# Kernel tuning notes

Measured on AMD Instinct MI355X. Metric: run time of the kernel, lower is better.

The kernel has to match this reference:

```python
import jax, jax.numpy as jnp
import numpy as np

NORM = 1.0  # normalization_factor


def _glorot(key, shape):
    fan_in, fan_out = shape
    lim = float(np.sqrt(6.0 / (fan_in + fan_out)))
    return jax.random.uniform(key, shape, jnp.float32, -lim, lim)


def setup_inputs() -> dict:
    key = jax.random.key(0)
    ks = jax.random.split(key, 12)
    B, N = 8, 2048
    latent, hidden, out_dim = 64, 128, 64
    inp = {
        "latent_features": jax.random.normal(ks[0], (B, N, latent), jnp.float32),
        "adjacency_matrix": jax.random.uniform(ks[1], (B, N, N), jnp.float32),
        "node_mask": jnp.ones((B, N, 1), jnp.float32),
        # 3 GCN layers: latent->hidden, hidden->hidden, hidden->hidden
        "W0": _glorot(ks[2], (latent, hidden)), "b0": jnp.zeros((hidden,), jnp.float32),
        "W1": _glorot(ks[3], (hidden, hidden)), "b1": jnp.zeros((hidden,), jnp.float32),
        "W2": _glorot(ks[4], (hidden, hidden)), "b2": jnp.zeros((hidden,), jnp.float32),
        # output projection hidden->out_dim
        "Wout": _glorot(ks[5], (hidden, out_dim)), "bout": jnp.zeros((out_dim,), jnp.float32),
    }
    return inp


def _gcn_layer(h, adj, W, b):
    # message transform (linear), gather+sum aggregate via dense adjacency, ReLU act
    msg = h @ W + b                      # [B,N,dout]
    agg = jnp.einsum('bij,bjd->bid', adj, msg) / NORM  # sum aggregation over neighbors
    return jax.nn.relu(agg)


def reference(latent_features, adjacency_matrix, node_mask,
              W0, b0, W1, b1, W2, b2, Wout, bout):
    h = _gcn_layer(latent_features, adjacency_matrix, W0, b0)
    h = _gcn_layer(h, adjacency_matrix, W1, b1)
    h = _gcn_layer(h, adjacency_matrix, W2, b2)
    # output projection + node mask
    return (h @ Wout + bout) * node_mask
```

## Files before the change

kernel.cpp:

```cpp
#include <hip/hip_runtime.h>
#include <hip/hip_bf16.h>


typedef __bf16 bf16;
typedef __bf16 bf16x4 __attribute__((ext_vector_type(4)));
typedef __bf16 bf16x8 __attribute__((ext_vector_type(8)));
typedef float  f32x16 __attribute__((ext_vector_type(16)));
typedef float  f32x4  __attribute__((ext_vector_type(4)));

static __device__ inline f32x16 mfma32(bf16x8 a, bf16x8 b, f32x16 c) {
    return __builtin_amdgcn_mfma_f32_32x32x16_bf16(a, b, c, 0, 0, 0);
}

#define NB   8
#define NN   2048
#define LAT  64
#define HID  128
#define ODIM 64

__global__ __launch_bounds__(256) void prep_t0_k(
    const float* __restrict__ lat, const float* __restrict__ W0,
    const float* __restrict__ b0,
    const float* __restrict__ W1, const float* __restrict__ W2,
    const float* __restrict__ Wout,
    bf16* __restrict__ msgT, bf16* __restrict__ WT1,
    bf16* __restrict__ WT2, bf16* __restrict__ WoutT)
{
    __shared__ __align__(16) bf16 WTs[HID * 72];
    int tid = threadIdx.x;
    int blk = blockIdx.x;

    if (blk >= 256) {
        int i = (blk - 256) * 256 + tid;
        if (i < HID * HID) { int fo = i >> 7, k = i & 127; WT1[i] = (bf16)W1[k * HID + fo]; return; }
        i -= HID * HID;
        if (i < HID * HID) { int fo = i >> 7, k = i & 127; WT2[i] = (bf16)W2[k * HID + fo]; return; }
        i -= HID * HID;
        if (i < ODIM * HID) { int o = i >> 7, k = i & 127; WoutT[i] = (bf16)Wout[k * ODIM + o]; return; }
        return;
    }

    for (int i = tid; i < LAT * HID; i += 256) {
        int k = i >> 7, fo = i & 127;
        WTs[fo * 72 + k] = (bf16)W0[i];
    }
    __syncthreads();

    int l = tid & 63, w = tid >> 6;
    int lm = l & 31, lh = l >> 5;
    int g0 = blk * 64;
    int b  = g0 >> 11, nb = g0 & 2047;

    const bf16*  Wrow = &WTs[(w * 32 + lm) * 72 + lh * 8];
    const float* r0   = lat + (size_t)(g0 + lm) * LAT + lh * 8;
    const float* r1   = r0 + (size_t)32 * LAT;

    f32x16 acc0 = {}, acc1 = {};
#pragma unroll
    for (int k0 = 0; k0 < LAT; k0 += 16) {
        bf16x8 a = *(const bf16x8*)(Wrow + k0);
        f32x4 x0 = *(const f32x4*)(r0 + k0), x1 = *(const f32x4*)(r0 + k0 + 4);
        f32x4 y0 = *(const f32x4*)(r1 + k0), y1 = *(const f32x4*)(r1 + k0 + 4);
        bf16x8 v0, v1;
        v0[0]=(bf16)x0[0]; v0[1]=(bf16)x0[1]; v0[2]=(bf16)x0[2]; v0[3]=(bf16)x0[3];
        v0[4]=(bf16)x1[0]; v0[5]=(bf16)x1[1]; v0[6]=(bf16)x1[2]; v0[7]=(bf16)x1[3];
        v1[0]=(bf16)y0[0]; v1[1]=(bf16)y0[1]; v1[2]=(bf16)y0[2]; v1[3]=(bf16)y0[3];
        v1[4]=(bf16)y1[0]; v1[5]=(bf16)y1[1]; v1[6]=(bf16)y1[2]; v1[7]=(bf16)y1[3];
        acc0 = mfma32(a, v0, acc0);
        acc1 = mfma32(a, v1, acc1);
    }

    bf16* outb = msgT + (size_t)b * (HID * NN) + nb;
#pragma unroll
    for (int r = 0; r < 16; ++r) {
        int fo = w * 32 + (r & 3) + 8 * (r >> 2) + 4 * lh;
        float bv = b0[fo];
        outb[(size_t)fo * NN + lm]      = (bf16)(acc0[r] + bv);
        outb[(size_t)fo * NN + 32 + lm] = (bf16)(acc1[r] + bv);
    }
}

template<int MODE, int ADJW>
__global__ __launch_bounds__(256) void agg_k(
    const float* __restrict__ adjf, const bf16* __restrict__ adjbi,
    bf16* __restrict__ adjbo,
    const bf16* __restrict__ msgT, const bf16* __restrict__ WTn,
    const float* __restrict__ biasn, bf16* __restrict__ msg_out,
    const float* __restrict__ mask, float* __restrict__ out)
{
    __shared__ __align__(16) bf16 As[2][32 * 72];
    __shared__ __align__(16) bf16 Bs[2][128 * 72];
    __shared__ __align__(16) bf16 Hs[32 * 136];
    int tid = threadIdx.x;
    int l = tid & 63, w = tid >> 6;
    int lm = l & 31, lh = l >> 5;
    int b  = blockIdx.x & 7;
    int m0 = (blockIdx.x >> 3) * 32;

    const bf16* msgb = msgT + (size_t)b * (HID * NN);
    int br = tid >> 3, bc = (tid & 7) * 8;
    const bf16* bsrc = msgb + (size_t)br * NN + bc;

    int ar = tid >> 4, ac = (tid & 15) * 4;
    const float* asrc = (ADJW == 0) ? adjf + (size_t)b * NN * NN + (size_t)(m0 + ar) * NN + ac : nullptr;
    bf16* adst = (ADJW == 0) ? adjbo + (size_t)b * NN * NN + (size_t)(m0 + ar) * NN + ac : nullptr;
    int ar8 = tid >> 3, ac8 = (tid & 7) * 8;
    const bf16* asrcb = (ADJW == 1) ? adjbi + (size_t)b * NN * NN + (size_t)(m0 + ar8) * NN + ac8 : nullptr;

    f32x4  fa0[2], fa1[2];
    bf16x8 ba[2];
    bf16x8 pb[2][4];

    auto loadTile = [&](int set, int k) {
        if (ADJW == 0) {
            fa0[set] = *(const f32x4*)(asrc + k);
            fa1[set] = *(const f32x4*)(asrc + (size_t)16 * NN + k);
        } else {
            ba[set] = *(const bf16x8*)(asrcb + k);
        }
        pb[set][0] = *(const bf16x8*)(bsrc + k);
        pb[set][1] = *(const bf16x8*)(bsrc + (size_t)32 * NN + k);
        pb[set][2] = *(const bf16x8*)(bsrc + (size_t)64 * NN + k);
        pb[set][3] = *(const bf16x8*)(bsrc + (size_t)96 * NN + k);
    };
    auto storeTile = [&](int set, int buf, int k) {
        if (ADJW == 0) {
            bf16x4 v0, v1;
            v0[0]=(bf16)fa0[set][0]; v0[1]=(bf16)fa0[set][1]; v0[2]=(bf16)fa0[set][2]; v0[3]=(bf16)fa0[set][3];
            v1[0]=(bf16)fa1[set][0]; v1[1]=(bf16)fa1[set][1]; v1[2]=(bf16)fa1[set][2]; v1[3]=(bf16)fa1[set][3];
            *(bf16x4*)&As[buf][ar * 72 + ac]        = v0;
            *(bf16x4*)&As[buf][(ar + 16) * 72 + ac] = v1;
            *(bf16x4*)(adst + k)                    = v0;
            *(bf16x4*)(adst + (size_t)16 * NN + k)  = v1;
        } else {
            *(bf16x8*)&As[buf][ar8 * 72 + ac8] = ba[set];
        }
        *(bf16x8*)&Bs[buf][br * 72 + bc]        = pb[set][0];
        *(bf16x8*)&Bs[buf][(br + 32) * 72 + bc] = pb[set][1];
        *(bf16x8*)&Bs[buf][(br + 64) * 72 + bc] = pb[set][2];
        *(bf16x8*)&Bs[buf][(br + 96) * 72 + bc] = pb[set][3];
    };

    f32x16 acc = {};
    auto mfmaTile = [&](int buf) {
        const bf16* Ac = &As[buf][lm * 72 + lh * 8];
        const bf16* Bc = &Bs[buf][(w * 32 + lm) * 72 + lh * 8];
#pragma unroll
        for (int s = 0; s < 4; ++s)
            acc = mfma32(*(const bf16x8*)(Ac + s * 16), *(const bf16x8*)(Bc + s * 16), acc);
    };

    loadTile(0, 0);
    loadTile(1, 64);
    storeTile(0, 0, 0);
    __syncthreads();

#pragma unroll 1
    for (int kt = 0; kt < 32; kt += 2) {
        if (kt + 2 < 32) loadTile(0, (kt + 2) * 64);
        mfmaTile(0);
        storeTile(1, 1, (kt + 1) * 64);
        __syncthreads();
        if (kt + 3 < 32) loadTile(1, (kt + 3) * 64);
        mfmaTile(1);
        if (kt + 2 < 32) storeTile(0, 0, (kt + 2) * 64);
        __syncthreads();
    }

#pragma unroll
    for (int r = 0; r < 16; ++r) {
        int row = (r & 3) + 8 * (r >> 2) + 4 * lh;
        float v = acc[r];
        Hs[row * 136 + w * 32 + lm] = (bf16)(v > 0.f ? v : 0.f);
    }
    __syncthreads();

    if (MODE == 0) {
        const bf16* Arow = WTn + (size_t)(w * 32 + lm) * HID + lh * 8;
        const bf16* Brow = &Hs[lm * 136 + lh * 8];
        f32x16 acc2 = {};
#pragma unroll
        for (int s = 0; s < 8; ++s)
            acc2 = mfma32(*(const bf16x8*)(Arow + s * 16), *(const bf16x8*)(Brow + s * 16), acc2);
        bf16* outb = msg_out + (size_t)b * (HID * NN) + m0;
#pragma unroll
        for (int r = 0; r < 16; ++r) {
            int fo = w * 32 + (r & 3) + 8 * (r >> 2) + 4 * lh;
            outb[(size_t)fo * NN + lm] = (bf16)(acc2[r] + biasn[fo]);
        }
    } else {
        if (w < 2) {
            int ob = w * 32;
            const bf16* Arow = &Hs[lm * 136 + lh * 8];
            const bf16* Brow = WTn + (size_t)(ob + lm) * HID + lh * 8;
            f32x16 acc2 = {};
#pragma unroll
            for (int s = 0; s < 8; ++s)
                acc2 = mfma32(*(const bf16x8*)(Arow + s * 16), *(const bf16x8*)(Brow + s * 16), acc2);
            float bv = biasn[ob + lm];
#pragma unroll
            for (int r = 0; r < 16; ++r) {
                int node = (r & 3) + 8 * (r >> 2) + 4 * lh;
                int g = b * NN + m0 + node;
                out[(size_t)g * ODIM + ob + lm] = (acc2[r] + bv) * mask[g];
            }
        }
    }
}

extern "C" void kernel_launch(void* const* d_in, const int* in_sizes, int n_in,
                              void* d_out, int out_size, void* d_ws, size_t ws_size,
                              hipStream_t stream)
{
    const float* lat  = (const float*)d_in[0];
    const float* adj  = (const float*)d_in[1];
    const float* mask = (const float*)d_in[2];
    const float* W0   = (const float*)d_in[3];
    const float* b0   = (const float*)d_in[4];
    const float* W1   = (const float*)d_in[5];
    const float* b1   = (const float*)d_in[6];
    const float* W2   = (const float*)d_in[7];
    const float* b2   = (const float*)d_in[8];
    const float* Wout = (const float*)d_in[9];
    const float* bout = (const float*)d_in[10];
    float* out = (float*)d_out;

    char* ws = (char*)d_ws;
    bf16* msgA  = (bf16*)(ws + 0);
    bf16* msgB  = (bf16*)(ws + 4194304);
    bf16* adjbf = (bf16*)(ws + 8388608);
    bf16* WT1   = (bf16*)(ws + 75497472);
    bf16* WT2   = (bf16*)(ws + 75530240);
    bf16* WoutT = (bf16*)(ws + 75563008);

    prep_t0_k<<<416, 256, 0, stream>>>(lat, W0, b0, W1, W2, Wout, msgA, WT1, WT2, WoutT);

    agg_k<0, 0><<<512, 256, 0, stream>>>(adj, nullptr, adjbf, msgA, WT1, b1, msgB, nullptr, nullptr);
    agg_k<0, 1><<<512, 256, 0, stream>>>(nullptr, adjbf, nullptr, msgB, WT2, b2, msgA, nullptr, nullptr);
    agg_k<1, 1><<<512, 256, 0, stream>>>(nullptr, adjbf, nullptr, msgA, WoutT, bout, nullptr, mask, out);
}
```

Measured before the change: 284.4 us.

## Load msg operand directly to registers, enlarge K chunk to 256

The aggregation kernel stops staging the transposed message operand through shared memory. Each wave now loads its B fragments straight from global memory into registers. Only the adjacency tile is double-buffered in LDS, with a larger K chunk (256) and fewer barriers, and the launch bounds request 3 blocks per CU. This removes the LDS traffic and syncs for the B operand, but it adds uncoalesced-ish global loads that depend on L2 reuse of msgT and raises register pressure.

```diff
diff --git a/kernel.cpp b/kernel.cpp
--- a/kernel.cpp
+++ b/kernel.cpp
@@ -3,7 +3,6 @@
 
 
 typedef __bf16 bf16;
-typedef __bf16 bf16x4 __attribute__((ext_vector_type(4)));
 typedef __bf16 bf16x8 __attribute__((ext_vector_type(8)));
 typedef float  f32x16 __attribute__((ext_vector_type(16)));
 typedef float  f32x4  __attribute__((ext_vector_type(4)));
@@ -81,16 +80,18 @@
 }
 
 template<int MODE, int ADJW>
-__global__ __launch_bounds__(256) void agg_k(
+__global__ __launch_bounds__(256, 3) void agg_k(
     const float* __restrict__ adjf, const bf16* __restrict__ adjbi,
     bf16* __restrict__ adjbo,
     const bf16* __restrict__ msgT, const bf16* __restrict__ WTn,
     const float* __restrict__ biasn, bf16* __restrict__ msg_out,
     const float* __restrict__ mask, float* __restrict__ out)
 {
-    __shared__ __align__(16) bf16 As[2][32 * 72];
-    __shared__ __align__(16) bf16 Bs[2][128 * 72];
+    constexpr int BKC = 256;
+    constexpr int SA  = 264;
+    __shared__ __align__(16) bf16 As[2][32 * SA];
     __shared__ __align__(16) bf16 Hs[32 * 136];
+
     int tid = threadIdx.x;
     int l = tid & 63, w = tid >> 6;
     int lm = l & 31, lh = l >> 5;
@@ -98,79 +99,69 @@
     int m0 = (blockIdx.x >> 3) * 32;
 
     const bf16* msgb = msgT + (size_t)b * (HID * NN);
-    int br = tid >> 3, bc = (tid & 7) * 8;
-    const bf16* bsrc = msgb + (size_t)br * NN + bc;
-
-    int ar = tid >> 4, ac = (tid & 15) * 4;
-    const float* asrc = (ADJW == 0) ? adjf + (size_t)b * NN * NN + (size_t)(m0 + ar) * NN + ac : nullptr;
-    bf16* adst = (ADJW == 0) ? adjbo + (size_t)b * NN * NN + (size_t)(m0 + ar) * NN + ac : nullptr;
-    int ar8 = tid >> 3, ac8 = (tid & 7) * 8;
-    const bf16* asrcb = (ADJW == 1) ? adjbi + (size_t)b * NN * NN + (size_t)(m0 + ar8) * NN + ac8 : nullptr;
-
-    f32x4  fa0[2], fa1[2];
-    bf16x8 ba[2];
-    bf16x8 pb[2][4];
-
-    auto loadTile = [&](int set, int k) {
+    const bf16* bsrc = msgb + (size_t)(w * 32 + lm) * NN + lh * 8;
+
+    int r = tid >> 3, c0 = (tid & 7) * 32;
+    const float* af  = (ADJW == 0) ? adjf  + (size_t)b * NN * NN + (size_t)(m0 + r) * NN + c0 : nullptr;
+    bf16*        awb = (ADJW == 0) ? adjbo + (size_t)b * NN * NN + (size_t)(m0 + r) * NN + c0 : nullptr;
+    const bf16*  ab  = (ADJW == 1) ? adjbi + (size_t)b * NN * NN + (size_t)(m0 + r) * NN + c0 : nullptr;
+
+    f32x4  fa[8];
+    bf16x8 ba[4];
+
+    auto loadA = [&](int k0) {
         if (ADJW == 0) {
-            fa0[set] = *(const f32x4*)(asrc + k);
-            fa1[set] = *(const f32x4*)(asrc + (size_t)16 * NN + k);
+#pragma unroll
+            for (int i = 0; i < 8; ++i) fa[i] = *(const f32x4*)(af + k0 + i * 4);
         } else {
-            ba[set] = *(const bf16x8*)(asrcb + k);
-        }
-        pb[set][0] = *(const bf16x8*)(bsrc + k);
-        pb[set][1] = *(const bf16x8*)(bsrc + (size_t)32 * NN + k);
-        pb[set][2] = *(const bf16x8*)(bsrc + (size_t)64 * NN + k);
-        pb[set][3] = *(const bf16x8*)(bsrc + (size_t)96 * NN + k);
+#pragma unroll
+            for (int i = 0; i < 4; ++i) ba[i] = *(const bf16x8*)(ab + k0 + i * 8);
+        }
     };
-    auto storeTile = [&](int set, int buf, int k) {
+    auto storeA = [&](int buf, int k0) {
         if (ADJW == 0) {
-            bf16x4 v0, v1;
-            v0[0]=(bf16)fa0[set][0]; v0[1]=(bf16)fa0[set][1]; v0[2]=(bf16)fa0[set][2]; v0[3]=(bf16)fa0[set][3];
-            v1[0]=(bf16)fa1[set][0]; v1[1]=(bf16)fa1[set][1]; v1[2]=(bf16)fa1[set][2]; v1[3]=(bf16)fa1[set][3];
-            *(bf16x4*)&As[buf][ar * 72 + ac]        = v0;
-            *(bf16x4*)&As[buf][(ar + 16) * 72 + ac] = v1;
-            *(bf16x4*)(adst + k)                    = v0;
-            *(bf16x4*)(adst + (size_t)16 * NN + k)  = v1;
+#pragma unroll
+            for (int i = 0; i < 4; ++i) {
+                bf16x8 v;
+                v[0]=(bf16)fa[2*i][0];   v[1]=(bf16)fa[2*i][1];
+                v[2]=(bf16)fa[2*i][2];   v[3]=(bf16)fa[2*i][3];
+                v[4]=(bf16)fa[2*i+1][0]; v[5]=(bf16)fa[2*i+1][1];
+                v[6]=(bf16)fa[2*i+1][2]; v[7]=(bf16)fa[2*i+1][3];
+                *(bf16x8*)&As[buf][r * SA + c0 + i * 8] = v;
+                *(bf16x8*)(awb + k0 + i * 8) = v;
+            }
         } else {
-            *(bf16x8*)&As[buf][ar8 * 72 + ac8] = ba[set];
-        }
-        *(bf16x8*)&Bs[buf][br * 72 + bc]        = pb[set][0];
-        *(bf16x8*)&Bs[buf][(br + 32) * 72 + bc] = pb[set][1];
-        *(bf16x8*)&Bs[buf][(br + 64) * 72 + bc] = pb[set][2];
-        *(bf16x8*)&Bs[buf][(br + 96) * 72 + bc] = pb[set][3];
+#pragma unroll
+            for (int i = 0; i < 4; ++i)
+                *(bf16x8*)&As[buf][r * SA + c0 + i * 8] = ba[i];
+        }
     };
 
     f32x16 acc = {};
-    auto mfmaTile = [&](int buf) {
-        const bf16* Ac = &As[buf][lm * 72 + lh * 8];
-        const bf16* Bc = &Bs[buf][(w * 32 + lm) * 72 + lh * 8];
-#pragma unroll
-        for (int s = 0; s < 4; ++s)
-            acc = mfma32(*(const bf16x8*)(Ac + s * 16), *(const bf16x8*)(Bc + s * 16), acc);
-    };
-
-    loadTile(0, 0);
-    loadTile(1, 64);
-    storeTile(0, 0, 0);
+    loadA(0);
+    storeA(0, 0);
     __syncthreads();
 
+    bf16x8 bb[16];
 #pragma unroll 1
-    for (int kt = 0; kt < 32; kt += 2) {
-        if (kt + 2 < 32) loadTile(0, (kt + 2) * 64);
-        mfmaTile(0);
-        storeTile(1, 1, (kt + 1) * 64);
+    for (int c = 0; c < 8; ++c) {
+        int cur = c & 1;
+        int k0 = c * BKC;
+#pragma unroll
+        for (int s = 0; s < 16; ++s) bb[s] = *(const bf16x8*)(bsrc + k0 + s * 16);
+        if (c < 7) loadA(k0 + BKC);
+        const bf16* Ac = &As[cur][lm * SA + lh * 8];
+#pragma unroll
+        for (int s = 0; s < 16; ++s)
+            acc = mfma32(*(const bf16x8*)(Ac + s * 16), bb[s], acc);
+        if (c < 7) storeA(cur ^ 1, k0 + BKC);
         __syncthreads();
-        if (kt + 3 < 32) loadTile(1, (kt + 3) * 64);
-        mfmaTile(1);
-        if (kt + 2 < 32) storeTile(0, 0, (kt + 2) * 64);
-        __syncthreads();
-    }
-
-#pragma unroll
-    for (int r = 0; r < 16; ++r) {
-        int row = (r & 3) + 8 * (r >> 2) + 4 * lh;
-        float v = acc[r];
+    }
+
+#pragma unroll
+    for (int rr = 0; rr < 16; ++rr) {
+        int row = (rr & 3) + 8 * (rr >> 2) + 4 * lh;
+        float v = acc[rr];
         Hs[row * 136 + w * 32 + lm] = (bf16)(v > 0.f ? v : 0.f);
     }
     __syncthreads();
@@ -184,9 +175,9 @@
             acc2 = mfma32(*(const bf16x8*)(Arow + s * 16), *(const bf16x8*)(Brow + s * 16), acc2);
         bf16* outb = msg_out + (size_t)b * (HID * NN) + m0;
 #pragma unroll
-        for (int r = 0; r < 16; ++r) {
-            int fo = w * 32 + (r & 3) + 8 * (r >> 2) + 4 * lh;
-            outb[(size_t)fo * NN + lm] = (bf16)(acc2[r] + biasn[fo]);
+        for (int rr = 0; rr < 16; ++rr) {
+            int fo = w * 32 + (rr & 3) + 8 * (rr >> 2) + 4 * lh;
+            outb[(size_t)fo * NN + lm] = (bf16)(acc2[rr] + biasn[fo]);
         }
     } else {
         if (w < 2) {
@@ -199,10 +190,10 @@
                 acc2 = mfma32(*(const bf16x8*)(Arow + s * 16), *(const bf16x8*)(Brow + s * 16), acc2);
             float bv = biasn[ob + lm];
 #pragma unroll
-            for (int r = 0; r < 16; ++r) {
-                int node = (r & 3) + 8 * (r >> 2) + 4 * lh;
+            for (int rr = 0; rr < 16; ++rr) {
+                int node = (rr & 3) + 8 * (rr >> 2) + 4 * lh;
                 int g = b * NN + m0 + node;
-                out[(size_t)g * ODIM + ob + lm] = (acc2[r] + bv) * mask[g];
+                out[(size_t)g * ODIM + ob + lm] = (acc2[rr] + bv) * mask[g];
             }
         }
     }
```

New measurement: 335.9 us. 1.18x slower.
